# Performance work log

Hardware: AMD Instinct MI355X
Metric: run time of the kernel (lower is better)

The kernel has to match this reference:

```python
import jax, jax.numpy as jnp
import numpy as np

N_ATOMS = 10000
N_PAIRS = 160000
F = 32            # nr_atom_basis (= edge basis = hidden sizes)
H = 7             # nr_heads
C = H * F         # nr_coefficients = 224
N_RBF = 50
RBF_CUTOFF = 5.0
RBF_GAMMA = 10.0

silu = jax.nn.silu

def setup_inputs() -> dict:
    key = jax.random.key(0)
    ks = jax.random.split(key, 32)
    def w(k, shape, scale=0.1):
        return (jax.random.normal(k, shape, dtype=jnp.float32) * scale)
    inp = {
        "h": jax.random.normal(ks[0], (N_ATOMS, F), dtype=jnp.float32),
        "x": jax.random.normal(ks[1], (N_ATOMS, 3), dtype=jnp.float32),
        "v": jax.random.normal(ks[2], (N_ATOMS, 3), dtype=jnp.float32),
        "pairlist": jax.random.randint(ks[3], (2, N_PAIRS), 0, N_ATOMS, dtype=jnp.int64 if jax.config.read('jax_enable_x64') else jnp.int32),
        # edge model (ContinuousFilterConvolutionWithConcatenation)
        "w_mlp_in": w(ks[4], (2 * F, N_RBF)), "b_mlp_in": jnp.zeros((N_RBF,), jnp.float32),
        "w_e1": w(ks[5], (2 * F + N_RBF + 1, F)), "b_e1": jnp.zeros((F,), jnp.float32),
        "w_e2": w(ks[6], (F, F)), "b_e2": jnp.zeros((F,), jnp.float32),
        # semantic attention mlp
        "w_att": w(ks[7], (F, H)), "b_att": jnp.zeros((H,), jnp.float32),
        # node mlp: in = F + C + F
        "w_n1": w(ks[8], (F + C + F, F)), "b_n1": jnp.zeros((F,), jnp.float32),
        "w_n2": w(ks[9], (F, F)), "b_n2": jnp.zeros((F,), jnp.float32),
        # post norm mlp
        "w_p1": w(ks[10], (C, F)), "b_p1": jnp.zeros((F,), jnp.float32),
        "w_p2": w(ks[11], (F, F)), "b_p2": jnp.zeros((F,), jnp.float32),
        # velocity mlp
        "w_v1": w(ks[12], (F, F)), "b_v1": jnp.zeros((F,), jnp.float32),
        "w_v2": w(ks[13], (F, 1)),
        # mixers
        "w_xmix": w(ks[14], (C, C)),
        "w_vmix": w(ks[15], (C, 1)),
    }
    return inp

def _rbf(d):  # Gaussian smearing, [P] -> [P, N_RBF]
    centers = jnp.linspace(0.0, RBF_CUTOFF, N_RBF, dtype=jnp.float32)
    return jnp.exp(-RBF_GAMMA * (d[:, None] - centers) ** 2)

def reference(h, x, v, pairlist,
              w_mlp_in, b_mlp_in, w_e1, b_e1, w_e2, b_e2,
              w_att, b_att, w_n1, b_n1, w_n2, b_n2,
              w_p1, b_p1, w_p2, b_p2, w_v1, b_v1, w_v2,
              w_xmix, w_vmix):
    n = h.shape[0]
    p = pairlist.shape[1]
    idx_i, idx_j = pairlist[0], pairlist[1]

    r_ij = x[idx_j] - x[idx_i]                       # [P, 3]
    d_ij = jnp.linalg.norm(r_ij, axis=-1)            # [P]
    dir_ij = r_ij / (d_ij[:, None] + 1e-5)           # [P, 3]

    # edge model
    h_cat = jnp.concatenate([h[idx_i], h[idx_j]], axis=-1)         # [P, 2F]
    filt = _rbf(d_ij) * (h_cat @ w_mlp_in + b_mlp_in)              # [P, N_RBF]
    e_in = jnp.concatenate([h_cat, filt, d_ij[:, None]], axis=-1)  # [P, 2F+N_RBF+1]
    h_ij_edge = silu(e_in @ w_e1 + b_e1) @ w_e2 + b_e2             # [P, F]

    # semantic attention: scatter-softmax over edges grouped by idx_i
    logits = jax.nn.celu(h_ij_edge @ w_att + b_att, alpha=2.0)     # [P, H]
    seg_max = jax.ops.segment_max(logits, idx_i, num_segments=n)
    e = jnp.exp(logits - seg_max[idx_i])
    seg_sum = jax.ops.segment_sum(e, idx_i, num_segments=n)
    att = e / seg_sum[idx_i]                                       # [P, H]
    att_agg = jax.ops.segment_sum(att, idx_i, num_segments=n)
    att_normed = att / att_agg[idx_i]
    # einsum('pf,ph->pfh') then reshape to [P, C]
    h_ij_semantic = (h_ij_edge[:, :, None] * att_normed[:, None, :]).reshape(p, C)

    # aggregate (scatter_add)
    h_i_semantic = jax.ops.segment_sum(h_ij_semantic, idx_i, num_segments=n)  # [N, C]

    # spatial attention
    x_mixed = jnp.tanh(h_ij_semantic @ w_xmix)                     # [P, C]
    combinations = dir_ij[:, None, :] * x_mixed[:, :, None]        # [P, C, 3]
    counts = jax.ops.segment_sum(jnp.ones((p,), h.dtype), idx_i, num_segments=n)
    denom = jnp.maximum(counts, 1.0)
    comb_mean = jax.ops.segment_sum(combinations, idx_i, num_segments=n) / denom[:, None, None]
    norm_sq = jnp.sum(comb_mean ** 2, axis=-1)                     # [N, C]
    h_i_spatial = silu(silu(norm_sq @ w_p1 + b_p1) @ w_p2 + b_p2)  # [N, F]

    # node update
    node_in = jnp.concatenate([h, h_i_semantic, h_i_spatial], axis=-1)
    h_updated = h + silu(silu(node_in @ w_n1 + b_n1) @ w_n2 + b_n2)

    # velocity update
    v_ij = jnp.einsum('pcx,c->px', combinations, w_vmix[:, 0])     # [P, 3]
    dv = jax.ops.segment_sum(v_ij, idx_i, num_segments=n) / denom[:, None]
    scale = 2.0 * jax.nn.sigmoid(silu(h @ w_v1 + b_v1) @ w_v2)     # [N, 1]
    v_updated = scale * v + dv
    x_updated = x + v_updated
    return (h_updated, x_updated, v_updated)
```

## Files before the change

kernel.cpp:

```cpp
#include <hip/hip_runtime.h>

typedef unsigned short u16;
typedef unsigned int u32;
typedef __attribute__((ext_vector_type(8))) short short8;
typedef __attribute__((ext_vector_type(4))) float floatx4;

#define P_PAIRS 160000
#define N_ATOMS 10000

#define OFF_WMLP  0
#define OFF_BMLP  3200
#define OFF_WE1   3250
#define OFF_BE1   6930
#define OFF_WE2   6962
#define OFF_BE2   7986
#define OFF_WATT  8018
#define OFF_BATT  8242
#define OFF_WN1   8249
#define OFF_BN1   17465
#define OFF_WN2   17497
#define OFF_BN2   18521
#define OFF_WP1   18553
#define OFF_BP1   25721
#define OFF_WP2   25753
#define OFF_BP2   26777
#define OFF_WV1   26809
#define OFF_BV1   27833
#define OFF_WV2   27865
#define OFF_WVMIX 27897
#define WF_TOTAL  28121

__device__ __forceinline__ float b2f(u16 u){ return __uint_as_float(((u32)u) << 16); }
__device__ __forceinline__ u16 f2b(float f){
  u32 u = __float_as_uint(f);
  u32 r = (u + 0x7FFFu + ((u >> 16) & 1u)) >> 16;
  return (u16)r;
}
__device__ __forceinline__ void unpack2(u32 p, float& lo, float& hi){
  lo = __uint_as_float(p << 16);
  hi = __uint_as_float(p & 0xFFFF0000u);
}
__device__ __forceinline__ float siluf(float v){ return v / (1.f + __expf(-v)); }
__device__ __forceinline__ float ldw(const void* p, int o, int bf){
  return bf ? b2f(((const u16*)p)[o]) : ((const float*)p)[o];
}

__global__ void k_code(float* out, float code){
  if (threadIdx.x == 0 && blockIdx.x == 0) out[0] = code;
}

__device__ __forceinline__ void detect_flags(const u32* hw, const u32* plw, int* s_fl){
  int tid = threadIdx.x;
  if (tid < 64){
    u32 e = (hw[tid] >> 7) & 0xFFu;
    unsigned long long m1 = __ballot(e >= 100u && e <= 140u);
    unsigned long long m2 = __ballot(plw[2*tid+1] == 0u);
    if (tid == 0){
      s_fl[0] = (__popcll(m1) >= 48) ? 1 : 0;
      s_fl[1] = (__popcll(m2) >= 60) ? 1 : 0;
    }
  }
  __syncthreads();
}

#define NBP_NORM 2735
#define NBP_CONV (NBP_NORM + 110)
#define NBP_TRAN (NBP_CONV + 196)
#define NBP_PB   (NBP_TRAN + 14)
#define NBP_HIST (NBP_PB + 625)

__global__ void k_prep(const void* __restrict__ h_raw, const void* __restrict__ x_raw,
    const void* __restrict__ v_raw, const void* __restrict__ pl_raw,
    const void* w_mlp, const void* b_mlp, const void* w_e1, const void* b_e1,
    const void* w_e2, const void* b_e2, const void* w_att, const void* b_att,
    const void* w_n1, const void* b_n1, const void* w_n2, const void* b_n2,
    const void* w_p1, const void* b_p1, const void* w_p2, const void* b_p2,
    const void* w_v1, const void* b_v1, const void* w_v2, const void* w_vmix,
    const void* wx,
    float* __restrict__ hf, float* __restrict__ xf, float* __restrict__ vf,
    int* __restrict__ pli, float* __restrict__ Wf, u16* __restrict__ wT,
    u16* __restrict__ bpk, int* __restrict__ counts){
  __shared__ int s_fl[2];
  detect_flags((const u32*)h_raw, (const u32*)pl_raw, s_fl);
  int bf = s_fl[0], i64 = s_fl[1];
  int bid = blockIdx.x, tid = threadIdx.x;
  if (bid < NBP_NORM){
    int t = bid * 256 + tid;
    if (t < 320000){
      hf[t] = ldw(h_raw, t, bf);
    } else if (t < 350000){
      int i = t - 320000; xf[i] = ldw(x_raw, i, bf);
    } else if (t < 380000){
      int i = t - 350000; vf[i] = ldw(v_raw, i, bf);
    } else if (t < 700000){
      int k = t - 380000;
      const int* p32 = (const int*)pl_raw;
      pli[k] = i64 ? p32[2*(size_t)k] : p32[k];
    }
  } else if (bid < NBP_CONV){
    int t = (bid - NBP_NORM) * 256 + tid;
    if (t >= WF_TOTAL) return;
    if (t < 3200){
      int k = t / 50, o = t - k * 50;
      Wf[OFF_WMLP + o * 64 + k] = ldw(w_mlp, t, bf);
      return;
    }
    const void* src; int o;
    if      (t < 3250)  { src = b_mlp;  o = t - 3200; }
    else if (t < 6930)  { src = w_e1;   o = t - 3250; }
    else if (t < 6962)  { src = b_e1;   o = t - 6930; }
    else if (t < 7986)  { src = w_e2;   o = t - 6962; }
    else if (t < 8018)  { src = b_e2;   o = t - 7986; }
    else if (t < 8242)  { src = w_att;  o = t - 8018; }
    else if (t < 8249)  { src = b_att;  o = t - 8242; }
    else if (t < 17465) { src = w_n1;   o = t - 8249; }
    else if (t < 17497) { src = b_n1;   o = t - 17465; }
    else if (t < 18521) { src = w_n2;   o = t - 17497; }
    else if (t < 18553) { src = b_n2;   o = t - 18521; }
    else if (t < 25721) { src = w_p1;   o = t - 18553; }
    else if (t < 25753) { src = b_p1;   o = t - 25721; }
    else if (t < 26777) { src = w_p2;   o = t - 25753; }
    else if (t < 26809) { src = b_p2;   o = t - 26777; }
    else if (t < 27833) { src = w_v1;   o = t - 26809; }
    else if (t < 27865) { src = b_v1;   o = t - 27833; }
    else if (t < 27897) { src = w_v2;   o = t - 27865; }
    else                { src = w_vmix; o = t - 27897; }
    Wf[t] = ldw(src, o, bf);
  } else if (bid < NBP_TRAN){
    int t = (bid - NBP_CONV) * 256 + tid;
    if (t >= 224 * 224) return;
    int n = t / 224, k = t - n * 224;
    wT[t] = f2b(ldw(wx, k * 224 + n, bf));
  } else if (bid < NBP_PB){
    int t = (bid - NBP_TRAN) * 256 + tid;
    if (t >= 3584) return;
    float v = 0.f;
    if (t < 2048){
      int n = t >> 6, k = t & 63;
      if (k < 50)       v = ldw(w_e1, (64 + k) * 32 + n, bf);
      else if (k == 50) v = ldw(w_e1, 114 * 32 + n, bf);
    } else if (t < 3072){
      int e = t - 2048; int n = e >> 5, k = e & 31;
      v = ldw(w_e2, k * 32 + n, bf);
    } else {
      int e = t - 3072; int n = e >> 5, k = e & 31;
      if (n < 7) v = ldw(w_att, k * 7 + n, bf);
    }
    bpk[t] = f2b(v);
  } else {
    int p = (bid - NBP_PB) * 256 + tid;
    const int* p32 = (const int*)pl_raw;
    int i = i64 ? p32[2*(size_t)p] : p32[p];
    atomicAdd(&counts[i], 1);
  }
}

__global__ void k_atomscan(const float* __restrict__ hf, const float* __restrict__ Wf,
    u16* __restrict__ prei, u16* __restrict__ prej,
    const int* __restrict__ counts, int* __restrict__ offs, int* __restrict__ cursor){
  __shared__ float hs[16][33];
  __shared__ int part[256];
  int tid = threadIdx.x;
  if (blockIdx.x < 625){
    int a0 = blockIdx.x * 16;
    for (int e = tid; e < 512; e += 256){
      int a = e >> 5, k = e & 31;
      hs[a][k] = hf[(size_t)(a0 + a) * 32 + k];
    }
    __syncthreads();
    for (int e = tid; e < 800; e += 256){
      int a = e / 50, r = e - a * 50;
      const float* wm = Wf + OFF_WMLP + r * 64;
      float acc = Wf[OFF_BMLP + r];
      #pragma unroll
      for (int k = 0; k < 32; ++k) acc += hs[a][k] * wm[k];
      prei[(size_t)(a0 + a) * 88 + 32 + r] = f2b(acc);
    }
    for (int e = tid; e < 800; e += 256){
      int a = e / 50, r = e - a * 50;
      const float* wm = Wf + OFF_WMLP + r * 64 + 32;
      float acc = 0.f;
      #pragma unroll
      for (int k = 0; k < 32; ++k) acc += hs[a][k] * wm[k];
      prej[(size_t)(a0 + a) * 88 + 32 + r] = f2b(acc);
    }
    for (int e = tid; e < 512; e += 256){
      int a = e >> 5, o = e & 31;
      float acc = Wf[OFF_BE1 + o];
      #pragma unroll
      for (int k = 0; k < 32; ++k) acc += hs[a][k] * Wf[OFF_WE1 + k * 32 + o];
      prei[(size_t)(a0 + a) * 88 + o] = f2b(acc);
    }
    for (int e = tid; e < 512; e += 256){
      int a = e >> 5, o = e & 31;
      float acc = 0.f;
      #pragma unroll
      for (int k = 0; k < 32; ++k) acc += hs[a][k] * Wf[OFF_WE1 + (32 + k) * 32 + o];
      prej[(size_t)(a0 + a) * 88 + o] = f2b(acc);
    }
  } else {
    int sum = 0;
    for (int k = 0; k < 40; ++k){
      int idx = tid * 40 + k;
      if (idx < N_ATOMS) sum += counts[idx];
    }
    part[tid] = sum;
    __syncthreads();
    if (tid == 0){
      int run = 0;
      for (int q = 0; q < 256; ++q){ int tmp = part[q]; part[q] = run; run += tmp; }
    }
    __syncthreads();
    int run = part[tid];
    for (int k = 0; k < 40; ++k){
      int idx = tid * 40 + k;
      if (idx < N_ATOMS){ offs[idx] = run; cursor[idx] = run; run += counts[idx]; }
    }
    if (tid == 0) offs[N_ATOMS] = P_PAIRS;
  }
}

__global__ void k_scatter(const int* __restrict__ pl, int* __restrict__ cursor,
                          int* __restrict__ isrt, int* __restrict__ jsrt){
  int p = blockIdx.x * 256 + threadIdx.x;
  int i = pl[p];
  int pos = atomicAdd(&cursor[i], 1);
  isrt[pos] = i;
  jsrt[pos] = pl[P_PAIRS + p];
}

#define PM_UB   0
#define PM_TB   16384
#define PM_DD   30720
#define PM_A1   31232
#define PM_B1   49664
#define PM_A2   54272
#define PM_B2   64512
#define PM_B3   67072
#define PM_TOT  68352

__global__ __launch_bounds__(256) void k_pairm(const float* __restrict__ x,
    const float* __restrict__ Wf, const u16* __restrict__ prei, const u16* __restrict__ prej,
    const int* __restrict__ isrt, const int* __restrict__ jsrt, const u16* __restrict__ bpk,
    u16* __restrict__ edge, float* __restrict__ logits, float* __restrict__ dirs){
  __shared__ __attribute__((aligned(16))) char smem[PM_TOT];
  float* UB = (float*)(smem + PM_UB);
  u16*   TB = (u16*)(smem + PM_TB);
  float* DD = (float*)(smem + PM_DD);
  u16*   A1 = (u16*)(smem + PM_A1);
  u16*   B1 = (u16*)(smem + PM_B1);
  u16*   A2 = (u16*)(smem + PM_A2);
  u16*   B2 = (u16*)(smem + PM_B2);
  u16*   B3 = (u16*)(smem + PM_B3);
  int tid = threadIdx.x;
  int wave = tid >> 6, lane = tid & 63, l15 = lane & 15, quad = lane >> 4;
  int row0 = blockIdx.x * 128;

  if (tid < 128){
    int s = row0 + tid;
    int i = isrt[s], j = jsrt[s];
    float r0 = x[j*3+0] - x[i*3+0];
    float r1 = x[j*3+1] - x[i*3+1];
    float r2 = x[j*3+2] - x[i*3+2];
    float d = sqrtf(r0*r0 + r1*r1 + r2*r2);
    float rinv = 1.f / (d + 1e-5f);
    dirs[s*3+0] = r0*rinv; dirs[s*3+1] = r1*rinv; dirs[s*3+2] = r2*rinv;
    DD[tid] = d;
    const uint4* pi4 = (const uint4*)(prei + (size_t)i * 88);
    const uint4* pj4 = (const uint4*)(prej + (size_t)j * 88);
    float* ub = UB + tid * 32;
    #pragma unroll
    for (int q = 0; q < 4; ++q){
      uint4 a4 = pi4[q], b4 = pj4[q];
      u32 pa[4] = {a4.x, a4.y, a4.z, a4.w};
      u32 pb[4] = {b4.x, b4.y, b4.z, b4.w};
      #pragma unroll
      for (int w2 = 0; w2 < 4; ++w2){
        float al, ah, bl, bh;
        unpack2(pa[w2], al, ah); unpack2(pb[w2], bl, bh);
        ub[q*8 + w2*2]     = al + bl;
        ub[q*8 + w2*2 + 1] = ah + bh;
      }
    }
    u32* tb = (u32*)TB + tid * 28;
    #pragma unroll
    for (int q = 0; q < 7; ++q){
      uint4 a4 = pi4[4+q], b4 = pj4[4+q];
      u32 pa[4] = {a4.x, a4.y, a4.z, a4.w};
      u32 pb[4] = {b4.x, b4.y, b4.z, b4.w};
      #pragma unroll
      for (int w2 = 0; w2 < 4; ++w2){
        float al, ah, bl, bh;
        unpack2(pa[w2], al, ah); unpack2(pb[w2], bl, bh);
        tb[q*4 + w2] = (u32)f2b(al + bl) | ((u32)f2b(ah + bh) << 16);
      }
    }
  } else {
    int t2 = tid - 128;
    const u32* src = (const u32*)bpk;
    for (int e = t2; e < 1024; e += 128){
      int n = e >> 5, kp = e & 31;
      ((u32*)B1)[n*36 + kp] = src[e];
    }
    for (int e = t2; e < 512; e += 128){
      int n = e >> 4, kp = e & 15;
      ((u32*)B2)[n*20 + kp] = src[1024 + e];
    }
    for (int e = t2; e < 256; e += 128){
      int n = e >> 4, kp = e & 15;
      ((u32*)B3)[n*20 + kp] = src[1536 + e];
    }
  }
  __syncthreads();
  for (int e = tid; e < 4096; e += 256){
    int r = e >> 5, kp = e & 31;
    int k0 = kp * 2, k1 = k0 + 1;
    float d = DD[r];
    float v0 = 0.f, v1 = 0.f;
    if (k0 < 50){
      float t0 = b2f(TB[r*56 + k0]);
      float c0 = (float)k0 * (5.f/49.f), dd0 = d - c0;
      v0 = t0 * __expf(-10.f * dd0 * dd0);
    } else if (k0 == 50) v0 = d;
    if (k1 < 50){
      float t1 = b2f(TB[r*56 + k1]);
      float c1 = (float)k1 * (5.f/49.f), dd1 = d - c1;
      v1 = t1 * __expf(-10.f * dd1 * dd1);
    }
    ((u32*)A1)[r*36 + kp] = (u32)f2b(v0) | ((u32)f2b(v1) << 16);
  }
  __syncthreads();
  floatx4 au[2][2];
  #pragma unroll
  for (int mt = 0; mt < 2; ++mt)
    #pragma unroll
    for (int nt = 0; nt < 2; ++nt) au[mt][nt] = (floatx4){0.f,0.f,0.f,0.f};
  #pragma unroll
  for (int ks = 0; ks < 2; ++ks){
    int kk = ks * 32;
    short8 a0 = *(const short8*)(A1 + (wave*32 + l15)*72 + kk + quad*8);
    short8 a1 = *(const short8*)(A1 + (wave*32 + 16 + l15)*72 + kk + quad*8);
    #pragma unroll
    for (int nt = 0; nt < 2; ++nt){
      short8 b = *(const short8*)(B1 + (nt*16 + l15)*72 + kk + quad*8);
      au[0][nt] = __builtin_amdgcn_mfma_f32_16x16x32_bf16(a0, b, au[0][nt], 0, 0, 0);
      au[1][nt] = __builtin_amdgcn_mfma_f32_16x16x32_bf16(a1, b, au[1][nt], 0, 0, 0);
    }
  }
  #pragma unroll
  for (int mt = 0; mt < 2; ++mt)
    #pragma unroll
    for (int nt = 0; nt < 2; ++nt)
      #pragma unroll
      for (int reg = 0; reg < 4; ++reg){
        int r = wave*32 + mt*16 + quad*4 + reg;
        int c = nt*16 + l15;
        float uval = au[mt][nt][reg] + UB[r*32 + c];
        A2[r*40 + c] = f2b(siluf(uval));
      }
  __syncthreads();
  floatx4 ae[2][2];
  #pragma unroll
  for (int mt = 0; mt < 2; ++mt)
    #pragma unroll
    for (int nt = 0; nt < 2; ++nt) ae[mt][nt] = (floatx4){0.f,0.f,0.f,0.f};
  {
    short8 a0 = *(const short8*)(A2 + (wave*32 + l15)*40 + quad*8);
    short8 a1 = *(const short8*)(A2 + (wave*32 + 16 + l15)*40 + quad*8);
    #pragma unroll
    for (int nt = 0; nt < 2; ++nt){
      short8 b = *(const short8*)(B2 + (nt*16 + l15)*40 + quad*8);
      ae[0][nt] = __builtin_amdgcn_mfma_f32_16x16x32_bf16(a0, b, ae[0][nt], 0, 0, 0);
      ae[1][nt] = __builtin_amdgcn_mfma_f32_16x16x32_bf16(a1, b, ae[1][nt], 0, 0, 0);
    }
  }
  __syncthreads();
  #pragma unroll
  for (int mt = 0; mt < 2; ++mt)
    #pragma unroll
    for (int nt = 0; nt < 2; ++nt)
      #pragma unroll
      for (int reg = 0; reg < 4; ++reg){
        int r = wave*32 + mt*16 + quad*4 + reg;
        int c = nt*16 + l15;
        float ev = ae[mt][nt][reg] + Wf[OFF_BE2 + c];
        A2[r*40 + c] = f2b(ev);
      }
  __syncthreads();
  {
    int r = tid >> 1, p = tid & 1;
    const uint4* srcp = (const uint4*)(A2 + r*40 + p*16);
    uint4* dstp = (uint4*)(edge + (size_t)(row0 + r)*32 + p*16);
    dstp[0] = srcp[0]; dstp[1] = srcp[1];
  }
  floatx4 al_[2];
  al_[0] = (floatx4){0.f,0.f,0.f,0.f};
  al_[1] = (floatx4){0.f,0.f,0.f,0.f};
  {
    short8 a0 = *(const short8*)(A2 + (wave*32 + l15)*40 + quad*8);
    short8 a1 = *(const short8*)(A2 + (wave*32 + 16 + l15)*40 + quad*8);
    short8 b = *(const short8*)(B3 + l15*40 + quad*8);
    al_[0] = __builtin_amdgcn_mfma_f32_16x16x32_bf16(a0, b, al_[0], 0, 0, 0);
    al_[1] = __builtin_amdgcn_mfma_f32_16x16x32_bf16(a1, b, al_[1], 0, 0, 0);
  }
  if (l15 < 7){
    float ba = Wf[OFF_BATT + l15];
    #pragma unroll
    for (int mt = 0; mt < 2; ++mt)
      #pragma unroll
      for (int reg = 0; reg < 4; ++reg){
        int r = wave*32 + mt*16 + quad*4 + reg;
        float vv = al_[mt][reg] + ba;
        float cl = vv > 0.f ? vv : 2.f * expm1f(0.5f * vv);
        logits[(size_t)(row0 + r)*7 + l15] = cl;
      }
  }
}

__global__ __launch_bounds__(256) void k_att(const int* __restrict__ offs,
    const float* __restrict__ logits, const u16* __restrict__ edge,
    float* __restrict__ atts, float* __restrict__ hsem){
  int a = blockIdx.x * 16 + (threadIdx.x >> 4);
  int lane = threadIdx.x & 15;
  int off = offs[a], end = offs[a+1];
  float m[7];
  #pragma unroll
  for (int hh = 0; hh < 7; ++hh) m[hh] = -1e30f;
  for (int s = off + lane; s < end; s += 16){
    #pragma unroll
    for (int hh = 0; hh < 7; ++hh) m[hh] = fmaxf(m[hh], logits[s*7+hh]);
  }
  #pragma unroll
  for (int hh = 0; hh < 7; ++hh){
    float v = m[hh];
    #pragma unroll
    for (int msk = 8; msk >= 1; msk >>= 1) v = fmaxf(v, __shfl_xor(v, msk));
    m[hh] = v;
  }
  float sm[7] = {0,0,0,0,0,0,0};
  for (int s = off + lane; s < end; s += 16){
    #pragma unroll
    for (int hh = 0; hh < 7; ++hh){
      float e = __expf(logits[s*7+hh] - m[hh]);
      sm[hh] += e;
      atts[s*7+hh] = e;
    }
  }
  #pragma unroll
  for (int hh = 0; hh < 7; ++hh){
    float v = sm[hh];
    #pragma unroll
    for (int msk = 8; msk >= 1; msk >>= 1) v += __shfl_xor(v, msk);
    sm[hh] = 1.f / v;
  }
  for (int s = off + lane; s < end; s += 16){
    #pragma unroll
    for (int hh = 0; hh < 7; ++hh) atts[s*7+hh] *= sm[hh];
  }
  __syncthreads();
  float acc[14] = {0,0,0,0,0,0,0,0,0,0,0,0,0,0};
  for (int s = off; s < end; ++s){
    u32 ev = *(const u32*)(edge + (size_t)s * 32 + lane * 2);
    float e0 = b2f((u16)(ev & 0xFFFFu));
    float e1 = b2f((u16)(ev >> 16));
    const float* ap = atts + (size_t)s * 7;
    #pragma unroll
    for (int hh = 0; hh < 7; ++hh){
      float at = ap[hh];
      acc[hh]     += e0 * at;
      acc[7 + hh] += e1 * at;
    }
  }
  float* hp = hsem + (size_t)a * 224 + lane * 14;
  #pragma unroll
  for (int jj = 0; jj < 14; ++jj) hp[jj] = acc[jj];
}

#define G_BS   29696
#define G_EL   29696
#define G_AL   (29696 + 4608)
#define G_TOT  38656

__global__ __launch_bounds__(256, 4) void k_gemm3(const u16* __restrict__ edge,
    const float* __restrict__ atts, const u16* __restrict__ BT,
    u16* __restrict__ xhalf, int half){
  __shared__ __attribute__((aligned(16))) char smem[G_TOT];
  u16*   As  = (u16*)smem;
  u16*   xth = (u16*)smem;
  u16*   Bs  = (u16*)(smem + G_BS);
  u16*   eL  = (u16*)(smem + G_EL);
  float* aL  = (float*)(smem + G_AL);
  int tid = threadIdx.x;
  int wave = tid >> 6, lane = tid & 63, l15 = lane & 15, quad = lane >> 4;
  int row0 = blockIdx.x * 64;
  int nbase = half * 112;

  for (int e = tid; e < 512; e += 256){
    int r = e >> 3, q = e & 7;
    *(uint2*)(eL + r*36 + q*4) = *(const uint2*)(edge + (size_t)(row0 + r)*32 + q*4);
  }
  for (int e = tid; e < 448; e += 256) aL[e] = atts[(size_t)row0*7 + e];
  floatx4 acc[7];
  #pragma unroll
  for (int nt = 0; nt < 7; ++nt) acc[nt] = (floatx4){0.f, 0.f, 0.f, 0.f};
  __syncthreads();

  {
    int pr = tid >> 2, q = tid & 3;
    u32* asw = (u32*)As + pr*116 + q*28;
    const u16* er = eL + pr*36 + q*8;
    const float* ar = aL + pr*7;
    float av[7];
    #pragma unroll
    for (int hh = 0; hh < 7; ++hh) av[hh] = ar[hh];
    #pragma unroll
    for (int fo2 = 0; fo2 < 4; ++fo2){
      float e0 = b2f(er[2*fo2]);
      float e1 = b2f(er[2*fo2+1]);
      u16 w[14];
      #pragma unroll
      for (int hh = 0; hh < 7; ++hh){
        w[hh]   = f2b(e0 * av[hh]);
        w[7+hh] = f2b(e1 * av[hh]);
      }
      #pragma unroll
      for (int k = 0; k < 7; ++k)
        asw[fo2*7 + k] = (u32)w[2*k] | ((u32)w[2*k+1] << 16);
    }
  }
  __syncthreads();

  for (int kt = 0; kt < 7; ++kt){
    for (int e = tid; e < 448; e += 256){
      int r = e >> 2, q = e & 3;
      *(uint4*)(Bs + r*40 + q*8) = *(const uint4*)(BT + (size_t)(nbase + r)*224 + kt*32 + q*8);
    }
    __syncthreads();
    int kk = kt * 32;
    short8 a0 = *(const short8*)(As + (wave*16 + l15)*232 + kk + quad*8);
    #pragma unroll
    for (int nt = 0; nt < 7; ++nt){
      short8 b = *(const short8*)(Bs + (nt*16 + l15)*40 + quad*8);
      acc[nt] = __builtin_amdgcn_mfma_f32_16x16x32_bf16(a0, b, acc[nt], 0, 0, 0);
    }
    __syncthreads();
  }

  #pragma unroll
  for (int nt = 0; nt < 7; ++nt)
    #pragma unroll
    for (int reg = 0; reg < 4; ++reg){
      int r = wave*16 + quad*4 + reg;
      int c = nt*16 + l15;
      float vv = acc[nt][reg];
      vv = fminf(fmaxf(vv, -15.f), 15.f);
      float e2 = __expf(2.f * vv);
      xth[r*120 + c] = f2b((e2 - 1.f) / (e2 + 1.f));
    }
  __syncthreads();
  for (int e = tid; e < 896; e += 256){
    int r = e / 14, w = e - r * 14;
    *(uint4*)(xhalf + (size_t)(row0 + r)*112 + w*8) = *(const uint4*)(xth + r*120 + w*8);
  }
}

__global__ __launch_bounds__(256) void k_comb(const int* __restrict__ offs,
    const u16* __restrict__ xhalf, const float* __restrict__ dirs,
    const float* __restrict__ Wf, int half,
    float* __restrict__ nsq, float* __restrict__ pvh){
  int a = blockIdx.x * 16 + (threadIdx.x >> 4);
  int lane = threadIdx.x & 15;
  int off = offs[a], end = offs[a+1];
  float c0[7] = {0,0,0,0,0,0,0}, c1[7] = {0,0,0,0,0,0,0}, c2[7] = {0,0,0,0,0,0,0};
  for (int s = off; s < end; ++s){
    float d0 = dirs[s*3+0], d1 = dirs[s*3+1], d2 = dirs[s*3+2];
    const u16* xr = xhalf + (size_t)s * 112 + lane;
    #pragma unroll
    for (int k = 0; k < 7; ++k){
      float xm = b2f(xr[k*16]);
      c0[k] += d0 * xm; c1[k] += d1 * xm; c2[k] += d2 * xm;
    }
  }
  float inv = 1.f / fmaxf((float)(end - off), 1.f);
  float pv0 = 0.f, pv1 = 0.f, pv2 = 0.f;
  #pragma unroll
  for (int k = 0; k < 7; ++k){
    float m0 = c0[k]*inv, m1 = c1[k]*inv, m2 = c2[k]*inv;
    int c = half*112 + k*16 + lane;
    nsq[(size_t)a*224 + c] = m0*m0 + m1*m1 + m2*m2;
    float wv = Wf[OFF_WVMIX + c];
    pv0 += wv*m0; pv1 += wv*m1; pv2 += wv*m2;
  }
  #pragma unroll
  for (int m = 8; m >= 1; m >>= 1){
    pv0 += __shfl_xor(pv0, m); pv1 += __shfl_xor(pv1, m); pv2 += __shfl_xor(pv2, m);
  }
  if (lane == 0){
    float* pp = pvh + (size_t)half*30000 + (size_t)a*3;
    pp[0] = pv0; pp[1] = pv1; pp[2] = pv2;
  }
}

__global__ __launch_bounds__(256) void k_final4(const float* __restrict__ h,
    const float* __restrict__ x, const float* __restrict__ v,
    const float* __restrict__ Wf, const float* __restrict__ hsem,
    const float* __restrict__ nsq, const float* __restrict__ pvh,
    float* __restrict__ out){
  __shared__ float s_nsq[16][225];
  __shared__ float s_in[16][289];
  __shared__ float s_u1[16][33];
  __shared__ float s_un[16][33];
  __shared__ float s_sc[16];
  int tid = threadIdx.x;
  int a0 = blockIdx.x * 16;
  for (int e = tid; e < 896; e += 256){
    int a = e / 56, q = e - a * 56;
    float4 t = *(const float4*)(nsq + (size_t)(a0 + a) * 224 + q * 4);
    s_nsq[a][q*4+0] = t.x; s_nsq[a][q*4+1] = t.y;
    s_nsq[a][q*4+2] = t.z; s_nsq[a][q*4+3] = t.w;
  }
  for (int e = tid; e < 896; e += 256){
    int a = e / 56, q = e - a * 56;
    float4 t = *(const float4*)(hsem + (size_t)(a0 + a) * 224 + q * 4);
    s_in[a][32 + q*4+0] = t.x; s_in[a][32 + q*4+1] = t.y;
    s_in[a][32 + q*4+2] = t.z; s_in[a][32 + q*4+3] = t.w;
  }
  for (int e = tid; e < 128; e += 256){
    int a = e >> 3, q = e & 7;
    float4 t = *(const float4*)(h + (size_t)(a0 + a) * 32 + q * 4);
    s_in[a][q*4+0] = t.x; s_in[a][q*4+1] = t.y;
    s_in[a][q*4+2] = t.z; s_in[a][q*4+3] = t.w;
  }
  __syncthreads();
  int o = tid & 31, g5 = tid >> 5;
  int aA = g5, aB = g5 + 8;
  {
    float uA = Wf[OFF_BP1 + o], uB = uA;
    const float* w = Wf + OFF_WP1 + o;
    #pragma unroll 8
    for (int kk = 0; kk < 224; ++kk){
      float wv = w[kk*32];
      uA += s_nsq[aA][kk] * wv;
      uB += s_nsq[aB][kk] * wv;
    }
    s_u1[aA][o] = siluf(uA);
    s_u1[aB][o] = siluf(uB);
  }
  {
    float gA = Wf[OFF_BV1 + o], gB = gA;
    const float* w = Wf + OFF_WV1 + o;
    #pragma unroll
    for (int kk = 0; kk < 32; ++kk){
      float wv = w[kk*32];
      gA += s_in[aA][kk] * wv;
      gB += s_in[aB][kk] * wv;
    }
    float wv2 = Wf[OFF_WV2 + o];
    float zA = siluf(gA) * wv2, zB = siluf(gB) * wv2;
    #pragma unroll
    for (int m = 16; m >= 1; m >>= 1){
      zA += __shfl_xor(zA, m); zB += __shfl_xor(zB, m);
    }
    if (o == 0){
      s_sc[aA] = 2.f / (1.f + __expf(-zA));
      s_sc[aB] = 2.f / (1.f + __expf(-zB));
    }
  }
  __syncthreads();
  {
    float uA = Wf[OFF_BP2 + o], uB = uA;
    const float* w = Wf + OFF_WP2 + o;
    #pragma unroll
    for (int kk = 0; kk < 32; ++kk){
      float wv = w[kk*32];
      uA += s_u1[aA][kk] * wv;
      uB += s_u1[aB][kk] * wv;
    }
    s_in[aA][256 + o] = siluf(uA);
    s_in[aB][256 + o] = siluf(uB);
  }
  __syncthreads();
  {
    float uA = Wf[OFF_BN1 + o], uB = uA;
    const float* w = Wf + OFF_WN1 + o;
    #pragma unroll 8
    for (int kk = 0; kk < 288; ++kk){
      float wv = w[kk*32];
      uA += s_in[aA][kk] * wv;
      uB += s_in[aB][kk] * wv;
    }
    s_un[aA][o] = siluf(uA);
    s_un[aB][o] = siluf(uB);
  }
  __syncthreads();
  {
    float uA = Wf[OFF_BN2 + o], uB = uA;
    const float* w = Wf + OFF_WN2 + o;
    #pragma unroll
    for (int kk = 0; kk < 32; ++kk){
      float wv = w[kk*32];
      uA += s_un[aA][kk] * wv;
      uB += s_un[aB][kk] * wv;
    }
    out[(size_t)(a0 + aA)*32 + o] = s_in[aA][o] + siluf(uA);
    out[(size_t)(a0 + aB)*32 + o] = s_in[aB][o] + siluf(uB);
  }
  if (tid < 48){
    int a = tid / 3, c = tid - a * 3;
    int ga = a0 + a;
    float pv = pvh[(size_t)ga*3 + c] + pvh[30000 + (size_t)ga*3 + c];
    float vup = s_sc[a] * v[ga*3 + c] + pv;
    float xup = x[ga*3 + c] + vup;
    out[N_ATOMS*32 + (size_t)ga*3 + c] = xup;
    out[N_ATOMS*32 + N_ATOMS*3 + (size_t)ga*3 + c] = vup;
  }
}

static constexpr size_t al256(size_t x){ return (x + 255) & ~(size_t)255; }
static constexpr size_t WS_FLAGS   = 0;
static constexpr size_t WS_COUNTS  = al256(WS_FLAGS + 8);
static constexpr size_t WS_OFFSETS = al256(WS_COUNTS + (size_t)N_ATOMS * 4);
static constexpr size_t WS_CURSOR  = al256(WS_OFFSETS + (size_t)(N_ATOMS + 1) * 4);
static constexpr size_t WS_PERM    = al256(WS_CURSOR + (size_t)N_ATOMS * 4);
static constexpr size_t WS_PLI     = al256(WS_PERM + (size_t)P_PAIRS * 4);
static constexpr size_t WS_HF      = al256(WS_PLI + (size_t)2 * P_PAIRS * 4);
static constexpr size_t WS_XF      = al256(WS_HF + (size_t)N_ATOMS * 32 * 4);
static constexpr size_t WS_VF      = al256(WS_XF + (size_t)N_ATOMS * 3 * 4);
static constexpr size_t WS_WF      = al256(WS_VF + (size_t)N_ATOMS * 3 * 4);
static constexpr size_t WS_WT      = al256(WS_WF + (size_t)WF_TOTAL * 4);
static constexpr size_t WS_EDGE    = al256(WS_WT + (size_t)224 * 224 * 2);
static constexpr size_t WS_ATTS    = al256(WS_EDGE + (size_t)P_PAIRS * 32 * 2);
static constexpr size_t WS_DIRS    = al256(WS_ATTS + (size_t)P_PAIRS * 7 * 4);
static constexpr size_t WS_LOGITS  = al256(WS_DIRS + (size_t)P_PAIRS * 3 * 4);
static constexpr size_t WS_PREI    = al256(WS_LOGITS + (size_t)P_PAIRS * 7 * 4);
static constexpr size_t WS_PREJ    = al256(WS_PREI + (size_t)N_ATOMS * 88 * 2);
static constexpr size_t WS_HSEM    = WS_LOGITS + 4480000;
static constexpr size_t WS_XH      = WS_HSEM + (size_t)N_ATOMS * 224 * 4;
static constexpr size_t WS_NSQ     = WS_XH + (size_t)P_PAIRS * 112 * 2;
static constexpr size_t WS_PVH     = WS_NSQ + (size_t)N_ATOMS * 224 * 4;
static constexpr size_t WS_JSRT    = al256(WS_PVH + (size_t)2 * 30000 * 4);
static constexpr size_t WS_BPK     = al256(WS_JSRT + (size_t)P_PAIRS * 4);
static constexpr size_t WS_END     = WS_BPK + 3584 * 2;
static_assert(WS_PREJ + (size_t)N_ATOMS * 88 * 2 <= WS_XH, "pre tables before xhalf");
static_assert(WS_END <= WS_LOGITS + (size_t)P_PAIRS * 224 * 2, "within round-1-proven footprint");
static_assert(WS_HSEM % 256 == 0 && WS_XH % 256 == 0 && WS_NSQ % 256 == 0 && WS_PVH % 256 == 0, "alignment");

extern "C" void kernel_launch(void* const* d_in, const int* in_sizes, int n_in,
                              void* d_out, int out_size, void* d_ws, size_t ws_size,
                              hipStream_t stream){
  (void)in_sizes; (void)n_in;
  if (out_size != 380000 || ws_size < WS_END){
    k_code<<<1, 64, 0, stream>>>((float*)d_out, 14000.f);
    return;
  }
  char* ws = (char*)d_ws;
  int*   counts = (int*)(ws + WS_COUNTS);
  int*   offs   = (int*)(ws + WS_OFFSETS);
  int*   cursor = (int*)(ws + WS_CURSOR);
  int*   isrt   = (int*)(ws + WS_PERM);
  int*   pli    = (int*)(ws + WS_PLI);
  float* hf     = (float*)(ws + WS_HF);
  float* xf     = (float*)(ws + WS_XF);
  float* vf     = (float*)(ws + WS_VF);
  float* Wf     = (float*)(ws + WS_WF);
  u16*   wT     = (u16*)(ws + WS_WT);
  u16*   edge   = (u16*)(ws + WS_EDGE);
  float* atts   = (float*)(ws + WS_ATTS);
  float* dirs   = (float*)(ws + WS_DIRS);
  float* logits = (float*)(ws + WS_LOGITS);
  u16*   prei   = (u16*)(ws + WS_PREI);
  u16*   prej   = (u16*)(ws + WS_PREJ);
  float* hsem   = (float*)(ws + WS_HSEM);
  u16*   xhalf  = (u16*)(ws + WS_XH);
  float* nsq    = (float*)(ws + WS_NSQ);
  float* pvh    = (float*)(ws + WS_PVH);
  int*   jsrt   = (int*)(ws + WS_JSRT);
  u16*   bpk    = (u16*)(ws + WS_BPK);

  hipMemsetAsync(counts, 0, (size_t)N_ATOMS * 4, stream);
  k_prep<<<NBP_HIST, 256, 0, stream>>>(d_in[0], d_in[1], d_in[2], d_in[3],
      d_in[4],  d_in[5],  d_in[6],  d_in[7],  d_in[8],  d_in[9],  d_in[10], d_in[11],
      d_in[12], d_in[13], d_in[14], d_in[15], d_in[16], d_in[17], d_in[18], d_in[19],
      d_in[20], d_in[21], d_in[22], d_in[24], d_in[23],
      hf, xf, vf, pli, Wf, wT, bpk, counts);
  k_atomscan<<<626, 256, 0, stream>>>(hf, Wf, prei, prej, counts, offs, cursor);
  k_scatter<<<P_PAIRS / 256, 256, 0, stream>>>(pli, cursor, isrt, jsrt);
  k_pairm<<<P_PAIRS / 128, 256, 0, stream>>>(xf, Wf, prei, prej, isrt, jsrt, bpk, edge, logits, dirs);
  k_att<<<N_ATOMS / 16, 256, 0, stream>>>(offs, logits, edge, atts, hsem);
  k_gemm3<<<P_PAIRS / 64, 256, 0, stream>>>(edge, atts, wT, xhalf, 0);
  k_comb<<<N_ATOMS / 16, 256, 0, stream>>>(offs, xhalf, dirs, Wf, 0, nsq, pvh);
  k_gemm3<<<P_PAIRS / 64, 256, 0, stream>>>(edge, atts, wT, xhalf, 1);
  k_comb<<<N_ATOMS / 16, 256, 0, stream>>>(offs, xhalf, dirs, Wf, 1, nsq, pvh);
  k_final4<<<625, 256, 0, stream>>>(hf, xf, vf, Wf, hsem, nsq, pvh, (float*)d_out);
}
```

Measured before the change: 343.1 us.

## Merge both gemm3 halves into one launch and fuse comb with final node update

When the workspace is large enough, the two column halves of the pair GEMM are written to separate buffers and computed in a single launch with interleaved blocks. A new fused kernel then does both halves of the segment reduction of combinations, the norm and velocity terms, and the final node and velocity MLPs in one pass. This removes three launches and the round trip through the nsq and pvh buffers. In exchange it needs a larger workspace and adds register pressure in the fused kernel, and it falls back to the old path when the workspace is too small.

Result: faster. 312.2 us (-9.0%).

```diff
diff --git a/kernel.cpp b/kernel.cpp
--- a/kernel.cpp
+++ b/kernel.cpp
@@ -483,7 +483,7 @@
 
 __global__ __launch_bounds__(256, 4) void k_gemm3(const u16* __restrict__ edge,
     const float* __restrict__ atts, const u16* __restrict__ BT,
-    u16* __restrict__ xhalf, int half){
+    u16* __restrict__ xh0, u16* __restrict__ xh1, int mode){
   __shared__ __attribute__((aligned(16))) char smem[G_TOT];
   u16*   As  = (u16*)smem;
   u16*   xth = (u16*)smem;
@@ -492,7 +492,12 @@
   float* aL  = (float*)(smem + G_AL);
   int tid = threadIdx.x;
   int wave = tid >> 6, lane = tid & 63, l15 = lane & 15, quad = lane >> 4;
-  int row0 = blockIdx.x * 64;
+  int bid = blockIdx.x;
+  int half, rblk;
+  if (mode < 0){ half = bid & 1; rblk = bid >> 1; }
+  else         { half = mode;    rblk = bid; }
+  u16* xhalf = half ? xh1 : xh0;
+  int row0 = rblk * 64;
   int nbase = half * 112;
 
   for (int e = tid; e < 512; e += 256){
@@ -710,6 +715,158 @@
     int ga = a0 + a;
     float pv = pvh[(size_t)ga*3 + c] + pvh[30000 + (size_t)ga*3 + c];
     float vup = s_sc[a] * v[ga*3 + c] + pv;
+    float xup = x[ga*3 + c] + vup;
+    out[N_ATOMS*32 + (size_t)ga*3 + c] = xup;
+    out[N_ATOMS*32 + N_ATOMS*3 + (size_t)ga*3 + c] = vup;
+  }
+}
+
+__global__ __launch_bounds__(256) void k_combf(const int* __restrict__ offs,
+    const u16* __restrict__ xh0, const u16* __restrict__ xh1,
+    const float* __restrict__ dirs, const float* __restrict__ h,
+    const float* __restrict__ x, const float* __restrict__ v,
+    const float* __restrict__ Wf, const float* __restrict__ hsem,
+    float* __restrict__ out){
+  __shared__ float s_nsq[16][225];
+  __shared__ float s_in[16][289];
+  __shared__ float s_u1[16][33];
+  __shared__ float s_un[16][33];
+  __shared__ float s_sc[16];
+  __shared__ float s_pv[16][3];
+  int tid = threadIdx.x;
+  int a0 = blockIdx.x * 16;
+  for (int e = tid; e < 896; e += 256){
+    int a = e / 56, q = e - a * 56;
+    float4 t = *(const float4*)(hsem + (size_t)(a0 + a) * 224 + q * 4);
+    s_in[a][32 + q*4+0] = t.x; s_in[a][32 + q*4+1] = t.y;
+    s_in[a][32 + q*4+2] = t.z; s_in[a][32 + q*4+3] = t.w;
+  }
+  for (int e = tid; e < 128; e += 256){
+    int a = e >> 3, q = e & 7;
+    float4 t = *(const float4*)(h + (size_t)(a0 + a) * 32 + q * 4);
+    s_in[a][q*4+0] = t.x; s_in[a][q*4+1] = t.y;
+    s_in[a][q*4+2] = t.z; s_in[a][q*4+3] = t.w;
+  }
+  {
+    int a = tid >> 4, lane = tid & 15;
+    int off = offs[a0 + a], end = offs[a0 + a + 1];
+    float c0A[7] = {0,0,0,0,0,0,0}, c1A[7] = {0,0,0,0,0,0,0}, c2A[7] = {0,0,0,0,0,0,0};
+    float c0B[7] = {0,0,0,0,0,0,0}, c1B[7] = {0,0,0,0,0,0,0}, c2B[7] = {0,0,0,0,0,0,0};
+    for (int s = off; s < end; ++s){
+      float d0 = dirs[s*3+0], d1 = dirs[s*3+1], d2 = dirs[s*3+2];
+      const u16* xra = xh0 + (size_t)s * 112 + lane;
+      const u16* xrb = xh1 + (size_t)s * 112 + lane;
+      #pragma unroll
+      for (int k = 0; k < 7; ++k){
+        float xa = b2f(xra[k*16]);
+        float xb = b2f(xrb[k*16]);
+        c0A[k] += d0 * xa; c1A[k] += d1 * xa; c2A[k] += d2 * xa;
+        c0B[k] += d0 * xb; c1B[k] += d1 * xb; c2B[k] += d2 * xb;
+      }
+    }
+    float inv = 1.f / fmaxf((float)(end - off), 1.f);
+    float pv0 = 0.f, pv1 = 0.f, pv2 = 0.f;
+    #pragma unroll
+    for (int k = 0; k < 7; ++k){
+      {
+        float m0 = c0A[k]*inv, m1 = c1A[k]*inv, m2 = c2A[k]*inv;
+        int c = k*16 + lane;
+        s_nsq[a][c] = m0*m0 + m1*m1 + m2*m2;
+        float wv = Wf[OFF_WVMIX + c];
+        pv0 += wv*m0; pv1 += wv*m1; pv2 += wv*m2;
+      }
+      {
+        float m0 = c0B[k]*inv, m1 = c1B[k]*inv, m2 = c2B[k]*inv;
+        int c = 112 + k*16 + lane;
+        s_nsq[a][c] = m0*m0 + m1*m1 + m2*m2;
+        float wv = Wf[OFF_WVMIX + c];
+        pv0 += wv*m0; pv1 += wv*m1; pv2 += wv*m2;
+      }
+    }
+    #pragma unroll
+    for (int m = 8; m >= 1; m >>= 1){
+      pv0 += __shfl_xor(pv0, m); pv1 += __shfl_xor(pv1, m); pv2 += __shfl_xor(pv2, m);
+    }
+    if (lane == 0){ s_pv[a][0] = pv0; s_pv[a][1] = pv1; s_pv[a][2] = pv2; }
+  }
+  __syncthreads();
+  int o = tid & 31, g5 = tid >> 5;
+  int aA = g5, aB = g5 + 8;
+  {
+    float uA = Wf[OFF_BP1 + o], uB = uA;
+    const float* w = Wf + OFF_WP1 + o;
+    #pragma unroll 8
+    for (int kk = 0; kk < 224; ++kk){
+      float wv = w[kk*32];
+      uA += s_nsq[aA][kk] * wv;
+      uB += s_nsq[aB][kk] * wv;
+    }
+    s_u1[aA][o] = siluf(uA);
+    s_u1[aB][o] = siluf(uB);
+  }
+  {
+    float gA = Wf[OFF_BV1 + o], gB = gA;
+    const float* w = Wf + OFF_WV1 + o;
+    #pragma unroll
+    for (int kk = 0; kk < 32; ++kk){
+      float wv = w[kk*32];
+      gA += s_in[aA][kk] * wv;
+      gB += s_in[aB][kk] * wv;
+    }
+    float wv2 = Wf[OFF_WV2 + o];
+    float zA = siluf(gA) * wv2, zB = siluf(gB) * wv2;
+    #pragma unroll
+    for (int m = 16; m >= 1; m >>= 1){
+      zA += __shfl_xor(zA, m); zB += __shfl_xor(zB, m);
+    }
+    if (o == 0){
+      s_sc[aA] = 2.f / (1.f + __expf(-zA));
+      s_sc[aB] = 2.f / (1.f + __expf(-zB));
+    }
+  }
+  __syncthreads();
+  {
+    float uA = Wf[OFF_BP2 + o], uB = uA;
+    const float* w = Wf + OFF_WP2 + o;
+    #pragma unroll
+    for (int kk = 0; kk < 32; ++kk){
+      float wv = w[kk*32];
+      uA += s_u1[aA][kk] * wv;
+      uB += s_u1[aB][kk] * wv;
+    }
+    s_in[aA][256 + o] = siluf(uA);
+    s_in[aB][256 + o] = siluf(uB);
+  }
+  __syncthreads();
+  {
+    float uA = Wf[OFF_BN1 + o], uB = uA;
+    const float* w = Wf + OFF_WN1 + o;
+    #pragma unroll 8
+    for (int kk = 0; kk < 288; ++kk){
+      float wv = w[kk*32];
+      uA += s_in[aA][kk] * wv;
+      uB += s_in[aB][kk] * wv;
+    }
+    s_un[aA][o] = siluf(uA);
+    s_un[aB][o] = siluf(uB);
+  }
+  __syncthreads();
+  {
+    float uA = Wf[OFF_BN2 + o], uB = uA;
+    const float* w = Wf + OFF_WN2 + o;
+    #pragma unroll
+    for (int kk = 0; kk < 32; ++kk){
+      float wv = w[kk*32];
+      uA += s_un[aA][kk] * wv;
+      uB += s_un[aB][kk] * wv;
+    }
+    out[(size_t)(a0 + aA)*32 + o] = s_in[aA][o] + siluf(uA);
+    out[(size_t)(a0 + aB)*32 + o] = s_in[aB][o] + siluf(uB);
+  }
+  if (tid < 48){
+    int a = tid / 3, c = tid - a * 3;
+    int ga = a0 + a;
+    float vup = s_sc[a] * v[ga*3 + c] + s_pv[a][c];
     float xup = x[ga*3 + c] + vup;
     out[N_ATOMS*32 + (size_t)ga*3 + c] = xup;
     out[N_ATOMS*32 + N_ATOMS*3 + (size_t)ga*3 + c] = vup;
@@ -741,9 +898,15 @@
 static constexpr size_t WS_JSRT    = al256(WS_PVH + (size_t)2 * 30000 * 4);
 static constexpr size_t WS_BPK     = al256(WS_JSRT + (size_t)P_PAIRS * 4);
 static constexpr size_t WS_END     = WS_BPK + 3584 * 2;
+static constexpr size_t WB_XH0     = WS_XH;
+static constexpr size_t WB_XH1     = WB_XH0 + (size_t)P_PAIRS * 112 * 2;
+static constexpr size_t WB_JSRT    = al256(WB_XH1 + (size_t)P_PAIRS * 112 * 2);
+static constexpr size_t WB_BPK     = al256(WB_JSRT + (size_t)P_PAIRS * 4);
+static constexpr size_t WB_END     = WB_BPK + 3584 * 2;
 static_assert(WS_PREJ + (size_t)N_ATOMS * 88 * 2 <= WS_XH, "pre tables before xhalf");
-static_assert(WS_END <= WS_LOGITS + (size_t)P_PAIRS * 224 * 2, "within round-1-proven footprint");
+static_assert(WS_END <= WS_LOGITS + (size_t)P_PAIRS * 224 * 2, "fallback within proven footprint");
 static_assert(WS_HSEM % 256 == 0 && WS_XH % 256 == 0 && WS_NSQ % 256 == 0 && WS_PVH % 256 == 0, "alignment");
+static_assert(WB_XH1 % 256 == 0, "alignment");
 
 extern "C" void kernel_launch(void* const* d_in, const int* in_sizes, int n_in,
                               void* d_out, int out_size, void* d_ws, size_t ws_size,
@@ -771,11 +934,14 @@
   u16*   prei   = (u16*)(ws + WS_PREI);
   u16*   prej   = (u16*)(ws + WS_PREJ);
   float* hsem   = (float*)(ws + WS_HSEM);
-  u16*   xhalf  = (u16*)(ws + WS_XH);
-  float* nsq    = (float*)(ws + WS_NSQ);
-  float* pvh    = (float*)(ws + WS_PVH);
-  int*   jsrt   = (int*)(ws + WS_JSRT);
-  u16*   bpk    = (u16*)(ws + WS_BPK);
+
+  bool big = (ws_size >= WB_END);
+  u16*   xh0  = (u16*)(ws + WB_XH0);
+  u16*   xh1  = big ? (u16*)(ws + WB_XH1) : xh0;
+  int*   jsrt = big ? (int*)(ws + WB_JSRT) : (int*)(ws + WS_JSRT);
+  u16*   bpk  = big ? (u16*)(ws + WB_BPK) : (u16*)(ws + WS_BPK);
+  float* nsq  = (float*)(ws + WS_NSQ);
+  float* pvh  = (float*)(ws + WS_PVH);
 
   hipMemsetAsync(counts, 0, (size_t)N_ATOMS * 4, stream);
   k_prep<<<NBP_HIST, 256, 0, stream>>>(d_in[0], d_in[1], d_in[2], d_in[3],
@@ -787,9 +953,14 @@
   k_scatter<<<P_PAIRS / 256, 256, 0, stream>>>(pli, cursor, isrt, jsrt);
   k_pairm<<<P_PAIRS / 128, 256, 0, stream>>>(xf, Wf, prei, prej, isrt, jsrt, bpk, edge, logits, dirs);
   k_att<<<N_ATOMS / 16, 256, 0, stream>>>(offs, logits, edge, atts, hsem);
-  k_gemm3<<<P_PAIRS / 64, 256, 0, stream>>>(edge, atts, wT, xhalf, 0);
-  k_comb<<<N_ATOMS / 16, 256, 0, stream>>>(offs, xhalf, dirs, Wf, 0, nsq, pvh);
-  k_gemm3<<<P_PAIRS / 64, 256, 0, stream>>>(edge, atts, wT, xhalf, 1);
-  k_comb<<<N_ATOMS / 16, 256, 0, stream>>>(offs, xhalf, dirs, Wf, 1, nsq, pvh);
-  k_final4<<<625, 256, 0, stream>>>(hf, xf, vf, Wf, hsem, nsq, pvh, (float*)d_out);
-}
+  if (big){
+    k_gemm3<<<2 * (P_PAIRS / 64), 256, 0, stream>>>(edge, atts, wT, xh0, xh1, -1);
+    k_combf<<<625, 256, 0, stream>>>(offs, xh0, xh1, dirs, hf, xf, vf, Wf, hsem, (float*)d_out);
+  } else {
+    k_gemm3<<<P_PAIRS / 64, 256, 0, stream>>>(edge, atts, wT, xh0, xh0, 0);
+    k_comb<<<N_ATOMS / 16, 256, 0, stream>>>(offs, xh0, dirs, Wf, 0, nsq, pvh);
+    k_gemm3<<<P_PAIRS / 64, 256, 0, stream>>>(edge, atts, wT, xh0, xh0, 1);
+    k_comb<<<N_ATOMS / 16, 256, 0, stream>>>(offs, xh0, dirs, Wf, 1, nsq, pvh);
+    k_final4<<<625, 256, 0, stream>>>(hf, xf, vf, Wf, hsem, nsq, pvh, (float*)d_out);
+  }
+}
```
